# Performance work log

Hardware: AMD Instinct MI355X
Metric: run time of the kernel (lower is better)

Reference implementation:

```python
import jax, jax.numpy as jnp
import numpy as np

HEADS = 8
HEAD_DIM = 64
GROUPS = 32
EPS = 1e-5


def setup_inputs() -> dict:
    key = jax.random.key(0)
    ks = jax.random.split(key, 8)
    B, C, H, W = 16, 256, 32, 32
    TD = 1024
    inner = HEADS * HEAD_DIM
    return {
        "x": jax.random.normal(ks[0], (B, C, H, W), jnp.float32),
        "embedding": jax.random.normal(ks[1], (B, TD), jnp.float32),
        "norm_w": jnp.ones((C,), jnp.float32),
        "norm_b": jnp.zeros((C,), jnp.float32),
        "in_w": jax.random.normal(ks[2], (3 * inner, C), jnp.float32) * (1.0 / np.sqrt(C)),
        "in_b": jnp.zeros((3 * inner,), jnp.float32),
        "out_w": jax.random.normal(ks[3], (C, inner), jnp.float32) * (1.0 / np.sqrt(inner)),
        "out_b": jnp.zeros((C,), jnp.float32),
        "emb_w": jax.random.normal(ks[4], (C, TD), jnp.float32) * (1.0 / np.sqrt(TD)),
        "emb_b": jnp.zeros((C,), jnp.float32),
    }


def reference(x, embedding, norm_w, norm_b, in_w, in_b, out_w, out_b, emb_w, emb_b):
    b, c, h, w = x.shape
    scale = 1.0 / np.sqrt(HEAD_DIM)
    # GroupNorm over (C//G, H, W) per group
    xg = x.reshape(b, GROUPS, -1)
    mean = xg.mean(-1, keepdims=True)
    var = xg.var(-1, keepdims=True)
    xn = ((xg - mean) * jax.lax.rsqrt(var + EPS)).reshape(b, c, h, w)
    xn = xn * norm_w[:, None, None] + norm_b[:, None, None]
    # 1x1 conv QKV projection: [b, 3*inner, h, w]
    qkv = jnp.einsum('oc,bchw->bohw', in_w, xn) + in_b[:, None, None]
    q, k, v = jnp.split(qkv, 3, axis=1)
    # [b, heads, head_dim, hw]
    q = q.reshape(b, HEADS, HEAD_DIM, h * w)
    k = k.reshape(b, HEADS, HEAD_DIM, h * w)
    v = v.reshape(b, HEADS, HEAD_DIM, h * w)
    attn = jax.nn.softmax(jnp.einsum('bhcm,bhcn->bhmn', q, k) * scale, axis=-1)
    o = jnp.einsum('bhmn,bhcn->bhcm', attn, v)  # [b,h,c,hw]
    o = o.reshape(b, HEADS * HEAD_DIM, h, w)
    out = jnp.einsum('oc,bchw->bohw', out_w, o) + out_b[:, None, None]
    emb = embedding @ emb_w.T + emb_b  # [b, C]
    return out * emb[:, :, None, None] + x
```

## Files before the change

### kernel.cpp

```cpp
#include <hip/hip_runtime.h>

#define DEV __device__ __forceinline__

typedef _Float16 f16;
typedef _Float16 f16x8 __attribute__((ext_vector_type(8)));
typedef _Float16 f16x4 __attribute__((ext_vector_type(4)));
typedef float f32x4 __attribute__((ext_vector_type(4)));

static constexpr int NB = 16;
static constexpr int NC = 256;
static constexpr int HW = 1024;
static constexpr int NG = 32;
static constexpr int CPG = 8;
static constexpr int NH = 8;
static constexpr int HD = 64;
static constexpr int INNER = 512;
static constexpr int TD = 1024;

DEV f32x4 mfma16(f16x8 a, f16x8 b, f32x4 c) {
    return __builtin_amdgcn_mfma_f32_16x16x32_f16(a, b, c, 0, 0, 0);
}

__global__ void gn_stats_k(const float* __restrict__ x, float* __restrict__ stats) {
    int bg = blockIdx.x;
    const float4* p = reinterpret_cast<const float4*>(x) + (size_t)bg * (CPG * HW / 4);
    float s = 0.f, ss = 0.f;
    for (int i = threadIdx.x; i < CPG * HW / 4; i += 256) {
        float4 v = p[i];
        s  += v.x + v.y + v.z + v.w;
        ss += v.x * v.x + v.y * v.y + v.z * v.z + v.w * v.w;
    }
    #pragma unroll
    for (int o = 32; o > 0; o >>= 1) {
        s  += __shfl_xor(s, o);
        ss += __shfl_xor(ss, o);
    }
    __shared__ float rs[4], rss[4];
    int wid = threadIdx.x >> 6;
    if ((threadIdx.x & 63) == 0) { rs[wid] = s; rss[wid] = ss; }
    __syncthreads();
    if (threadIdx.x == 0) {
        s  = rs[0] + rs[1] + rs[2] + rs[3];
        ss = rss[0] + rss[1] + rss[2] + rss[3];
        const float inv_n = 1.f / (float)(CPG * HW);
        float mean = s * inv_n;
        float var  = ss * inv_n - mean * mean;
        stats[bg * 2]     = mean;
        stats[bg * 2 + 1] = rsqrtf(var + 1e-5f);
    }
}

__global__ void gn_apply_k(const float* __restrict__ x, const float* __restrict__ stats,
                           const float* __restrict__ nw, const float* __restrict__ nb,
                           f16* __restrict__ xnT) {
    int b = blockIdx.y;
    int m = blockIdx.x * 256 + threadIdx.x;
    const float* xb = x + (size_t)b * NC * HW + m;
    f16* op = xnT + ((size_t)b * HW + m) * NC;
    for (int c0 = 0; c0 < NC; c0 += 4) {
        f16x4 h;
        #pragma unroll
        for (int j = 0; j < 4; ++j) {
            int c = c0 + j;
            float mean = stats[(b * NG + (c >> 3)) * 2];
            float rstd = stats[(b * NG + (c >> 3)) * 2 + 1];
            float v = xb[(size_t)c * HW];
            h[j] = (f16)(((v - mean) * rstd) * nw[c] + nb[c]);
        }
        *reinterpret_cast<f16x4*>(op + c0) = h;
    }
}

__global__ void conv_w_k(const float* __restrict__ a, const float* __restrict__ bw,
                         f16* __restrict__ wa, f16* __restrict__ wb) {
    int i = blockIdx.x * 256 + threadIdx.x;
    const int N1 = 3 * INNER * NC / 4;
    float4 v;
    f16* dst;
    if (i < N1) { v = reinterpret_cast<const float4*>(a)[i];      dst = wa + (size_t)i * 4; }
    else        { v = reinterpret_cast<const float4*>(bw)[i - N1]; dst = wb + (size_t)(i - N1) * 4; }
    f16x4 h4 = {(f16)v.x, (f16)v.y, (f16)v.z, (f16)v.w};
    *reinterpret_cast<f16x4*>(dst) = h4;
}

__global__ __launch_bounds__(256) void gemm_qkv_k(
        const f16* __restrict__ wA, const f16* __restrict__ xnT,
        const float* __restrict__ bias,
        f16* __restrict__ qT, f16* __restrict__ kT, f16* __restrict__ vv) {
    int b  = blockIdx.z;
    int o0 = blockIdx.x * 128;
    int m0 = blockIdx.y * 128;
    int wid  = threadIdx.x >> 6;
    int lane = threadIdx.x & 63;
    int wr = (wid >> 1) * 64, wc = (wid & 1) * 64;
    int lr = lane & 15, lg = lane >> 4;

    const f16* A  = wA  + (size_t)(o0 + wr + lr) * NC + lg * 8;
    const f16* Bp = xnT + ((size_t)b * HW + m0 + wc + lr) * NC + lg * 8;

    const f32x4 fzero = {0.f, 0.f, 0.f, 0.f};
    f32x4 acc[4][4];
    #pragma unroll
    for (int i = 0; i < 4; ++i) {
        #pragma unroll
        for (int j = 0; j < 4; ++j) acc[i][j] = fzero;
    }

    for (int k0 = 0; k0 < NC; k0 += 32) {
        f16x8 af[4], bf[4];
        #pragma unroll
        for (int i = 0; i < 4; ++i)
            af[i] = *reinterpret_cast<const f16x8*>(A + (size_t)i * 16 * NC + k0);
        #pragma unroll
        for (int j = 0; j < 4; ++j)
            bf[j] = *reinterpret_cast<const f16x8*>(Bp + (size_t)j * 16 * NC + k0);
        #pragma unroll
        for (int i = 0; i < 4; ++i) {
            #pragma unroll
            for (int j = 0; j < 4; ++j)
                acc[i][j] = mfma16(af[i], bf[j], acc[i][j]);
        }
    }

    #pragma unroll
    for (int i = 0; i < 4; ++i) {
        int ob = o0 + wr + i * 16 + lg * 4;
        #pragma unroll
        for (int j = 0; j < 4; ++j) {
            int m = m0 + wc + j * 16 + lr;
            float v0 = acc[i][j][0] + bias[ob];
            float v1 = acc[i][j][1] + bias[ob + 1];
            float v2 = acc[i][j][2] + bias[ob + 2];
            float v3 = acc[i][j][3] + bias[ob + 3];
            if (ob < INNER) {
                int h = ob >> 6, c = ob & 63;
                f16x4 pk = {(f16)v0, (f16)v1, (f16)v2, (f16)v3};
                *reinterpret_cast<f16x4*>(qT + (((size_t)(b * NH + h) * HW + m) * HD + c)) = pk;
            } else if (ob < 2 * INNER) {
                int oo = ob - INNER;
                int h = oo >> 6, c = oo & 63;
                f16x4 pk = {(f16)v0, (f16)v1, (f16)v2, (f16)v3};
                *reinterpret_cast<f16x4*>(kT + (((size_t)(b * NH + h) * HW + m) * HD + c)) = pk;
            } else {
                int oo = ob - 2 * INNER;
                int h = oo >> 6, c = oo & 63;
                f16* vp = vv + ((size_t)(b * NH + h) * HD + c) * HW + m;
                vp[0]      = (f16)v0;
                vp[HW]     = (f16)v1;
                vp[2 * HW] = (f16)v2;
                vp[3 * HW] = (f16)v3;
            }
        }
    }
}

__global__ void emb_gemm_k(const float* __restrict__ e, const float* __restrict__ ew,
                           const float* __restrict__ eb, float* __restrict__ embS) {
    int b = blockIdx.y;
    int co = blockIdx.x * 4 + (threadIdx.x >> 6);
    int lane = threadIdx.x & 63;
    const float4* ep = reinterpret_cast<const float4*>(e + (size_t)b * TD);
    const float4* wp = reinterpret_cast<const float4*>(ew + (size_t)co * TD);
    float s = 0.f;
    for (int t = lane; t < TD / 4; t += 64) {
        float4 a = ep[t], w = wp[t];
        s += a.x * w.x + a.y * w.y + a.z * w.z + a.w * w.w;
    }
    #pragma unroll
    for (int o = 32; o > 0; o >>= 1) s += __shfl_xor(s, o);
    if (lane == 0) embS[b * NC + co] = s + eb[co];
}

DEV void load_kv(const f16* __restrict__ kp, const f16* __restrict__ vp,
                 int n0, int lr, int lg, f16x8 (&kf)[2][2], f16x8 (&vf)[4]) {
    #pragma unroll
    for (int kt = 0; kt < 2; ++kt)
        #pragma unroll
        for (int ks2 = 0; ks2 < 2; ++ks2)
            kf[kt][ks2] = *reinterpret_cast<const f16x8*>(
                kp + (size_t)(n0 + kt * 16 + lr) * HD + ks2 * 32 + lg * 8);
    #pragma unroll
    for (int dt = 0; dt < 4; ++dt)
        vf[dt] = *reinterpret_cast<const f16x8*>(
            vp + (size_t)(dt * 16 + lr) * HW + n0 + lg * 8);
}

DEV void attn_tile(const f16x8 (&kf)[2][2], const f16x8 (&vf)[4],
                   const f16x8 (&qf)[4][2],
                   f32x4 (&oa)[4][4], float (&mr)[4], float (&lsl)[4],
                   f16 (&pl)[16][40], int lr, int lg) {
    const float sl = 0.125f * 1.44269504088896f;
    const float THR = 11.0f;
    const f32x4 fzero = {0.f, 0.f, 0.f, 0.f};
    #pragma unroll
    for (int qt = 0; qt < 4; ++qt) {
        f32x4 sc0 = fzero, sc1 = fzero;
        __builtin_amdgcn_s_setprio(1);
        sc0 = mfma16(kf[0][0], qf[qt][0], sc0);
        sc0 = mfma16(kf[0][1], qf[qt][1], sc0);
        sc1 = mfma16(kf[1][0], qf[qt][0], sc1);
        sc1 = mfma16(kf[1][1], qf[qt][1], sc1);
        __builtin_amdgcn_s_setprio(0);

        float a0 = fmaxf(fmaxf(sc0[0], sc0[1]), fmaxf(sc0[2], sc0[3]));
        float a1 = fmaxf(fmaxf(sc1[0], sc1[1]), fmaxf(sc1[2], sc1[3]));
        float pmax = fmaxf(a0, a1) * sl;
        if (__any(pmax - mr[qt] > THR)) {
            float pm = pmax;
            pm = fmaxf(pm, __shfl_xor(pm, 16));
            pm = fmaxf(pm, __shfl_xor(pm, 32));
            float mn = fmaxf(mr[qt], pm);
            float f = exp2f(mr[qt] - mn);
            mr[qt] = mn;
            lsl[qt] *= f;
            #pragma unroll
            for (int dt = 0; dt < 4; ++dt)
                #pragma unroll
                for (int r = 0; r < 4; ++r) oa[qt][dt][r] *= f;
        }
        float p[8];
        #pragma unroll
        for (int r = 0; r < 4; ++r) p[r]     = exp2f(fmaf(sc0[r], sl, -mr[qt]));
        #pragma unroll
        for (int r = 0; r < 4; ++r) p[4 + r] = exp2f(fmaf(sc1[r], sl, -mr[qt]));
        lsl[qt] += ((p[0] + p[1]) + (p[2] + p[3])) + ((p[4] + p[5]) + (p[6] + p[7]));

        f16x4 w0 = {(f16)p[0], (f16)p[1], (f16)p[2], (f16)p[3]};
        f16x4 w1 = {(f16)p[4], (f16)p[5], (f16)p[6], (f16)p[7]};
        *reinterpret_cast<f16x4*>(&pl[lr][lg * 4])      = w0;
        *reinterpret_cast<f16x4*>(&pl[lr][16 + lg * 4]) = w1;
        f16x8 pf = *reinterpret_cast<const f16x8*>(&pl[lr][lg * 8]);

        __builtin_amdgcn_s_setprio(1);
        #pragma unroll
        for (int dt = 0; dt < 4; ++dt)
            oa[qt][dt] = mfma16(vf[dt], pf, oa[qt][dt]);
        __builtin_amdgcn_s_setprio(0);
    }
}

__global__ __launch_bounds__(256) void attn_k(
        const f16* __restrict__ qT, const f16* __restrict__ kT, const f16* __restrict__ vv,
        f16* __restrict__ oT) {
    int u = ((blockIdx.x & 7) << 6) | (blockIdx.x >> 3);
    int bh = u >> 2;
    int mt = u & 3;
    int b = bh >> 3, h = bh & 7;
    int wid = threadIdx.x >> 6;
    int lane = threadIdx.x & 63;
    int lr = lane & 15, lg = lane >> 4;
    int mw = mt * 256 + wid * 64;

    const f16* qp = qT + (size_t)bh * HW * HD;
    const f16* kp = kT + (size_t)bh * HW * HD;
    const f16* vp = vv + (size_t)bh * HD * HW;

    __shared__ __align__(16) f16 pl[4][16][40];

    f16x8 qf[4][2];
    #pragma unroll
    for (int qt = 0; qt < 4; ++qt)
        #pragma unroll
        for (int ks2 = 0; ks2 < 2; ++ks2)
            qf[qt][ks2] = *reinterpret_cast<const f16x8*>(
                qp + (size_t)(mw + qt * 16 + lr) * HD + ks2 * 32 + lg * 8);

    const f32x4 fzero = {0.f, 0.f, 0.f, 0.f};
    f32x4 oa[4][4];
    #pragma unroll
    for (int qt = 0; qt < 4; ++qt)
        #pragma unroll
        for (int dt = 0; dt < 4; ++dt) oa[qt][dt] = fzero;
    float mr[4]  = {-1e30f, -1e30f, -1e30f, -1e30f};
    float lsl[4] = {0.f, 0.f, 0.f, 0.f};

    f16x8 kfA[2][2], vfA[4], kfB[2][2], vfB[4];
    load_kv(kp, vp, 0, lr, lg, kfA, vfA);
    for (int n0 = 0; n0 < HW; n0 += 64) {
        load_kv(kp, vp, n0 + 32, lr, lg, kfB, vfB);
        attn_tile(kfA, vfA, qf, oa, mr, lsl, pl[wid], lr, lg);
        if (n0 + 64 < HW) load_kv(kp, vp, n0 + 64, lr, lg, kfA, vfA);
        attn_tile(kfB, vfB, qf, oa, mr, lsl, pl[wid], lr, lg);
    }

    #pragma unroll
    for (int qt = 0; qt < 4; ++qt) {
        float t = lsl[qt];
        t += __shfl_xor(t, 16);
        t += __shfl_xor(t, 32);
        float inv = 1.f / t;
        int m = mw + qt * 16 + lr;
        f16* op = oT + ((size_t)b * HW + m) * INNER + h * HD;
        #pragma unroll
        for (int dt = 0; dt < 4; ++dt) {
            f16x4 o4;
            #pragma unroll
            for (int r = 0; r < 4; ++r) o4[r] = (f16)(oa[qt][dt][r] * inv);
            *reinterpret_cast<f16x4*>(op + dt * 16 + lg * 4) = o4;
        }
    }
}

__global__ __launch_bounds__(256) void gemm_out_k(
        const f16* __restrict__ wA, const f16* __restrict__ oT,
        const float* __restrict__ bias, const float* __restrict__ embS,
        const float* __restrict__ x, float* __restrict__ out) {
    int b  = blockIdx.z;
    int o0 = blockIdx.x * 128;
    int m0 = blockIdx.y * 128;
    int wid  = threadIdx.x >> 6;
    int lane = threadIdx.x & 63;
    int wr = (wid >> 1) * 64, wc = (wid & 1) * 64;
    int lr = lane & 15, lg = lane >> 4;

    const f16* A  = wA + (size_t)(o0 + wr + lr) * INNER + lg * 8;
    const f16* Bp = oT + ((size_t)b * HW + m0 + wc + lr) * INNER + lg * 8;

    const f32x4 fzero = {0.f, 0.f, 0.f, 0.f};
    f32x4 acc[4][4];
    #pragma unroll
    for (int i = 0; i < 4; ++i) {
        #pragma unroll
        for (int j = 0; j < 4; ++j) acc[i][j] = fzero;
    }

    for (int k0 = 0; k0 < INNER; k0 += 32) {
        f16x8 af[4], bf[4];
        #pragma unroll
        for (int i = 0; i < 4; ++i)
            af[i] = *reinterpret_cast<const f16x8*>(A + (size_t)i * 16 * INNER + k0);
        #pragma unroll
        for (int j = 0; j < 4; ++j)
            bf[j] = *reinterpret_cast<const f16x8*>(Bp + (size_t)j * 16 * INNER + k0);
        #pragma unroll
        for (int i = 0; i < 4; ++i) {
            #pragma unroll
            for (int j = 0; j < 4; ++j)
                acc[i][j] = mfma16(af[i], bf[j], acc[i][j]);
        }
    }

    #pragma unroll
    for (int i = 0; i < 4; ++i) {
        int ob = o0 + wr + i * 16 + lg * 4;
        #pragma unroll
        for (int j = 0; j < 4; ++j) {
            int m = m0 + wc + j * 16 + lr;
            #pragma unroll
            for (int r = 0; r < 4; ++r) {
                int o = ob + r;
                size_t idx = ((size_t)b * NC + o) * HW + m;
                out[idx] = (acc[i][j][r] + bias[o]) * embS[b * NC + o] + x[idx];
            }
        }
    }
}

extern "C" void kernel_launch(void* const* d_in, const int* in_sizes, int n_in,
                              void* d_out, int out_size, void* d_ws, size_t ws_size,
                              hipStream_t stream) {
    const float* x     = (const float*)d_in[0];
    const float* emb   = (const float*)d_in[1];
    const float* nw    = (const float*)d_in[2];
    const float* nbi   = (const float*)d_in[3];
    const float* in_w  = (const float*)d_in[4];
    const float* in_b  = (const float*)d_in[5];
    const float* out_w = (const float*)d_in[6];
    const float* out_b = (const float*)d_in[7];
    const float* emb_w = (const float*)d_in[8];
    const float* emb_b = (const float*)d_in[9];

    char* p = (char*)d_ws;
    f16* xnT   = (f16*)p;   p += (size_t)NB * HW * NC * 2;
    f16* w_in  = (f16*)p;   p += (size_t)3 * INNER * NC * 2;
    f16* w_out = (f16*)p;   p += (size_t)NC * INNER * 2;
    float* stats = (float*)p; p += (size_t)NB * NG * 2 * 4;
    float* embS  = (float*)p; p += (size_t)NB * NC * 4;
    f16* qT = (f16*)p;      p += (size_t)NB * NH * HW * HD * 2;
    f16* kT = (f16*)p;      p += (size_t)NB * NH * HW * HD * 2;
    f16* vv = (f16*)p;      p += (size_t)NB * NH * HW * HD * 2;
    f16* oT = (f16*)p;

    gn_stats_k<<<NB * NG, 256, 0, stream>>>(x, stats);
    gn_apply_k<<<dim3(HW / 256, NB), 256, 0, stream>>>(x, stats, nw, nbi, xnT);
    conv_w_k<<<512, 256, 0, stream>>>(in_w, out_w, w_in, w_out);
    gemm_qkv_k<<<dim3(12, 8, NB), 256, 0, stream>>>(w_in, xnT, in_b, qT, kT, vv);
    emb_gemm_k<<<dim3(NC / 4, NB), 256, 0, stream>>>(emb, emb_w, emb_b, embS);
    attn_k<<<512, 256, 0, stream>>>(qT, kT, vv, oT);
    gemm_out_k<<<dim3(NC / 128, HW / 128, NB), 256, 0, stream>>>(w_out, oT, out_b, embS, x, (float*)d_out);
}
```

Measured before the change: 178.4 us.

## Halve attention query rows per wave, fold softmax scale into K, MFMA row sums

The attention kernel now gives each wave 32 query rows instead of 64 and launches twice as many blocks. This cuts accumulator registers, which should allow more waves per SIMD, but K and V are re-read from memory twice as often. The softmax scale and log2e factor are applied to K in the QKV GEMM epilogue, so the per-element FMA goes away. Row sums are accumulated by an MFMA against a ones vector instead of VALU adds and shuffles, P is packed with cvt_pkrtz, and V loads drop to a single buffer.

```diff
diff --git a/kernel.cpp b/kernel.cpp
--- a/kernel.cpp
+++ b/kernel.cpp
@@ -6,6 +6,7 @@
 typedef _Float16 f16x8 __attribute__((ext_vector_type(8)));
 typedef _Float16 f16x4 __attribute__((ext_vector_type(4)));
 typedef float f32x4 __attribute__((ext_vector_type(4)));
+typedef unsigned int u32;
 
 static constexpr int NB = 16;
 static constexpr int NC = 256;
@@ -19,6 +20,11 @@
 
 DEV f32x4 mfma16(f16x8 a, f16x8 b, f32x4 c) {
     return __builtin_amdgcn_mfma_f32_16x16x32_f16(a, b, c, 0, 0, 0);
+}
+
+DEV u32 pk2(float a, float b) {
+    auto c = __builtin_amdgcn_cvt_pkrtz(a, b);
+    return __builtin_bit_cast(u32, c);
 }
 
 __global__ void gn_stats_k(const float* __restrict__ x, float* __restrict__ stats) {
@@ -122,6 +128,7 @@
         }
     }
 
+    const float SL = 0.18033688011112042f;
     #pragma unroll
     for (int i = 0; i < 4; ++i) {
         int ob = o0 + wr + i * 16 + lg * 4;
@@ -139,7 +146,7 @@
             } else if (ob < 2 * INNER) {
                 int oo = ob - INNER;
                 int h = oo >> 6, c = oo & 63;
-                f16x4 pk = {(f16)v0, (f16)v1, (f16)v2, (f16)v3};
+                f16x4 pk = {(f16)(v0 * SL), (f16)(v1 * SL), (f16)(v2 * SL), (f16)(v3 * SL)};
                 *reinterpret_cast<f16x4*>(kT + (((size_t)(b * NH + h) * HW + m) * HD + c)) = pk;
             } else {
                 int oo = ob - 2 * INNER;
@@ -171,29 +178,28 @@
     if (lane == 0) embS[b * NC + co] = s + eb[co];
 }
 
-DEV void load_kv(const f16* __restrict__ kp, const f16* __restrict__ vp,
-                 int n0, int lr, int lg, f16x8 (&kf)[2][2], f16x8 (&vf)[4]) {
-    #pragma unroll
-    for (int kt = 0; kt < 2; ++kt)
-        #pragma unroll
-        for (int ks2 = 0; ks2 < 2; ++ks2)
-            kf[kt][ks2] = *reinterpret_cast<const f16x8*>(
-                kp + (size_t)(n0 + kt * 16 + lr) * HD + ks2 * 32 + lg * 8);
+DEV void load_k(const f16* __restrict__ kpl, int n0, f16x8 (&kf)[2][2]) {
+    const f16* p0 = kpl + (size_t)n0 * HD;
+    kf[0][0] = *reinterpret_cast<const f16x8*>(p0);
+    kf[0][1] = *reinterpret_cast<const f16x8*>(p0 + 32);
+    kf[1][0] = *reinterpret_cast<const f16x8*>(p0 + 16 * HD);
+    kf[1][1] = *reinterpret_cast<const f16x8*>(p0 + 16 * HD + 32);
+}
+DEV void load_v(const f16* __restrict__ vpl, int n0, f16x8 (&vf)[4]) {
     #pragma unroll
     for (int dt = 0; dt < 4; ++dt)
-        vf[dt] = *reinterpret_cast<const f16x8*>(
-            vp + (size_t)(dt * 16 + lr) * HW + n0 + lg * 8);
+        vf[dt] = *reinterpret_cast<const f16x8*>(vpl + (size_t)dt * 16 * HW + n0);
 }
 
 DEV void attn_tile(const f16x8 (&kf)[2][2], const f16x8 (&vf)[4],
-                   const f16x8 (&qf)[4][2],
-                   f32x4 (&oa)[4][4], float (&mr)[4], float (&lsl)[4],
+                   const f16x8 (&qf)[2][2],
+                   f32x4 (&oa)[2][4], f32x4 (&lacc)[2], float (&mr)[2],
                    f16 (&pl)[16][40], int lr, int lg) {
-    const float sl = 0.125f * 1.44269504088896f;
     const float THR = 11.0f;
     const f32x4 fzero = {0.f, 0.f, 0.f, 0.f};
-    #pragma unroll
-    for (int qt = 0; qt < 4; ++qt) {
+    const f16x8 ones = {(f16)1, (f16)1, (f16)1, (f16)1, (f16)1, (f16)1, (f16)1, (f16)1};
+    #pragma unroll
+    for (int qt = 0; qt < 2; ++qt) {
         f32x4 sc0 = fzero, sc1 = fzero;
         __builtin_amdgcn_s_setprio(1);
         sc0 = mfma16(kf[0][0], qf[qt][0], sc0);
@@ -202,9 +208,9 @@
         sc1 = mfma16(kf[1][1], qf[qt][1], sc1);
         __builtin_amdgcn_s_setprio(0);
 
-        float a0 = fmaxf(fmaxf(sc0[0], sc0[1]), fmaxf(sc0[2], sc0[3]));
-        float a1 = fmaxf(fmaxf(sc1[0], sc1[1]), fmaxf(sc1[2], sc1[3]));
-        float pmax = fmaxf(a0, a1) * sl;
+        float m0 = fmaxf(fmaxf(sc0[0], sc0[1]), fmaxf(sc0[2], sc0[3]));
+        float m1 = fmaxf(fmaxf(sc1[0], sc1[1]), fmaxf(sc1[2], sc1[3]));
+        float pmax = fmaxf(m0, m1);
         if (__any(pmax - mr[qt] > THR)) {
             float pm = pmax;
             pm = fmaxf(pm, __shfl_xor(pm, 16));
@@ -212,7 +218,8 @@
             float mn = fmaxf(mr[qt], pm);
             float f = exp2f(mr[qt] - mn);
             mr[qt] = mn;
-            lsl[qt] *= f;
+            #pragma unroll
+            for (int r = 0; r < 4; ++r) lacc[qt][r] *= f;
             #pragma unroll
             for (int dt = 0; dt < 4; ++dt)
                 #pragma unroll
@@ -220,21 +227,23 @@
         }
         float p[8];
         #pragma unroll
-        for (int r = 0; r < 4; ++r) p[r]     = exp2f(fmaf(sc0[r], sl, -mr[qt]));
-        #pragma unroll
-        for (int r = 0; r < 4; ++r) p[4 + r] = exp2f(fmaf(sc1[r], sl, -mr[qt]));
-        lsl[qt] += ((p[0] + p[1]) + (p[2] + p[3])) + ((p[4] + p[5]) + (p[6] + p[7]));
-
-        f16x4 w0 = {(f16)p[0], (f16)p[1], (f16)p[2], (f16)p[3]};
-        f16x4 w1 = {(f16)p[4], (f16)p[5], (f16)p[6], (f16)p[7]};
-        *reinterpret_cast<f16x4*>(&pl[lr][lg * 4])      = w0;
-        *reinterpret_cast<f16x4*>(&pl[lr][16 + lg * 4]) = w1;
+        for (int r = 0; r < 4; ++r) p[r]     = exp2f(sc0[r] - mr[qt]);
+        #pragma unroll
+        for (int r = 0; r < 4; ++r) p[4 + r] = exp2f(sc1[r] - mr[qt]);
+
+        u32 w01[2] = {pk2(p[0], p[1]), pk2(p[2], p[3])};
+        u32 w23[2] = {pk2(p[4], p[5]), pk2(p[6], p[7])};
+        *reinterpret_cast<u32*>(&pl[lr][lg * 4])          = w01[0];
+        *reinterpret_cast<u32*>(&pl[lr][lg * 4 + 2])      = w01[1];
+        *reinterpret_cast<u32*>(&pl[lr][16 + lg * 4])     = w23[0];
+        *reinterpret_cast<u32*>(&pl[lr][16 + lg * 4 + 2]) = w23[1];
         f16x8 pf = *reinterpret_cast<const f16x8*>(&pl[lr][lg * 8]);
 
         __builtin_amdgcn_s_setprio(1);
         #pragma unroll
         for (int dt = 0; dt < 4; ++dt)
             oa[qt][dt] = mfma16(vf[dt], pf, oa[qt][dt]);
+        lacc[qt] = mfma16(ones, pf, lacc[qt]);
         __builtin_amdgcn_s_setprio(0);
     }
 }
@@ -242,53 +251,52 @@
 __global__ __launch_bounds__(256) void attn_k(
         const f16* __restrict__ qT, const f16* __restrict__ kT, const f16* __restrict__ vv,
         f16* __restrict__ oT) {
-    int u = ((blockIdx.x & 7) << 6) | (blockIdx.x >> 3);
-    int bh = u >> 2;
-    int mt = u & 3;
+    int u = ((blockIdx.x & 7) << 7) | (blockIdx.x >> 3);
+    int bh = u >> 3;
+    int mt = u & 7;
     int b = bh >> 3, h = bh & 7;
     int wid = threadIdx.x >> 6;
     int lane = threadIdx.x & 63;
     int lr = lane & 15, lg = lane >> 4;
-    int mw = mt * 256 + wid * 64;
-
-    const f16* qp = qT + (size_t)bh * HW * HD;
-    const f16* kp = kT + (size_t)bh * HW * HD;
-    const f16* vp = vv + (size_t)bh * HD * HW;
+    int mw = mt * 128 + wid * 32;
+
+    const f16* qp  = qT + (size_t)bh * HW * HD;
+    const f16* kpl = kT + (size_t)bh * HW * HD + lr * HD + lg * 8;
+    const f16* vpl = vv + (size_t)bh * HD * HW + lr * HW + lg * 8;
 
     __shared__ __align__(16) f16 pl[4][16][40];
 
-    f16x8 qf[4][2];
-    #pragma unroll
-    for (int qt = 0; qt < 4; ++qt)
+    f16x8 qf[2][2];
+    #pragma unroll
+    for (int qt = 0; qt < 2; ++qt)
         #pragma unroll
         for (int ks2 = 0; ks2 < 2; ++ks2)
             qf[qt][ks2] = *reinterpret_cast<const f16x8*>(
                 qp + (size_t)(mw + qt * 16 + lr) * HD + ks2 * 32 + lg * 8);
 
     const f32x4 fzero = {0.f, 0.f, 0.f, 0.f};
-    f32x4 oa[4][4];
-    #pragma unroll
-    for (int qt = 0; qt < 4; ++qt)
+    f32x4 oa[2][4];
+    f32x4 lacc[2] = {fzero, fzero};
+    #pragma unroll
+    for (int qt = 0; qt < 2; ++qt)
         #pragma unroll
         for (int dt = 0; dt < 4; ++dt) oa[qt][dt] = fzero;
-    float mr[4]  = {-1e30f, -1e30f, -1e30f, -1e30f};
-    float lsl[4] = {0.f, 0.f, 0.f, 0.f};
-
-    f16x8 kfA[2][2], vfA[4], kfB[2][2], vfB[4];
-    load_kv(kp, vp, 0, lr, lg, kfA, vfA);
+    float mr[2] = {-1e30f, -1e30f};
+
+    f16x8 kfA[2][2], kfB[2][2], vf[4];
+    load_k(kpl, 0, kfA);
     for (int n0 = 0; n0 < HW; n0 += 64) {
-        load_kv(kp, vp, n0 + 32, lr, lg, kfB, vfB);
-        attn_tile(kfA, vfA, qf, oa, mr, lsl, pl[wid], lr, lg);
-        if (n0 + 64 < HW) load_kv(kp, vp, n0 + 64, lr, lg, kfA, vfA);
-        attn_tile(kfB, vfB, qf, oa, mr, lsl, pl[wid], lr, lg);
-    }
-
-    #pragma unroll
-    for (int qt = 0; qt < 4; ++qt) {
-        float t = lsl[qt];
-        t += __shfl_xor(t, 16);
-        t += __shfl_xor(t, 32);
-        float inv = 1.f / t;
+        load_v(vpl, n0, vf);
+        load_k(kpl, n0 + 32, kfB);
+        attn_tile(kfA, vf, qf, oa, lacc, mr, pl[wid], lr, lg);
+        load_v(vpl, n0 + 32, vf);
+        if (n0 + 64 < HW) load_k(kpl, n0 + 64, kfA);
+        attn_tile(kfB, vf, qf, oa, lacc, mr, pl[wid], lr, lg);
+    }
+
+    #pragma unroll
+    for (int qt = 0; qt < 2; ++qt) {
+        float inv = 1.f / lacc[qt][0];
         int m = mw + qt * 16 + lr;
         f16* op = oT + ((size_t)b * HW + m) * INNER + h * HD;
         #pragma unroll
@@ -386,6 +394,6 @@
     conv_w_k<<<512, 256, 0, stream>>>(in_w, out_w, w_in, w_out);
     gemm_qkv_k<<<dim3(12, 8, NB), 256, 0, stream>>>(w_in, xnT, in_b, qT, kT, vv);
     emb_gemm_k<<<dim3(NC / 4, NB), 256, 0, stream>>>(emb, emb_w, emb_b, embS);
-    attn_k<<<512, 256, 0, stream>>>(qT, kT, vv, oT);
+    attn_k<<<1024, 256, 0, stream>>>(qT, kT, vv, oT);
     gemm_out_k<<<dim3(NC / 128, HW / 128, NB), 256, 0, stream>>>(w_out, oT, out_b, embS, x, (float*)d_out);
 }
```

After: 224.2 us. 25.7% more time.
